# Optimization experiments

Measured on AMD Instinct MI355X. Metric: run time of the kernel, lower is better.

The kernel has to match this reference:

```python
import jax, jax.numpy as jnp
import numpy as np

B, S, E = 2, 2048, 2048
H, W = 16, 256  # num_heads, window_size
D = E // H      # head_dim = 128


def setup_inputs() -> dict:
    key = jax.random.key(0)
    ks = jax.random.split(key, 9)
    s = 1.0 / np.sqrt(E)
    return {
        "x": jax.random.normal(ks[0], (B, S, E), dtype=jnp.float32),
        "Wq": jax.random.normal(ks[1], (E, E), dtype=jnp.float32) * s,
        "bq": jax.random.normal(ks[2], (E,), dtype=jnp.float32) * 0.01,
        "Wk": jax.random.normal(ks[3], (E, E), dtype=jnp.float32) * s,
        "bk": jax.random.normal(ks[4], (E,), dtype=jnp.float32) * 0.01,
        "Wv": jax.random.normal(ks[5], (E, E), dtype=jnp.float32) * s,
        "bv": jax.random.normal(ks[6], (E,), dtype=jnp.float32) * 0.01,
        "Wo": jax.random.normal(ks[7], (E, E), dtype=jnp.float32) * s,
        "bo": jax.random.normal(ks[8], (E,), dtype=jnp.float32) * 0.01,
    }


def reference(x, Wq, bq, Wk, bk, Wv, bv, Wo, bo):
    Bsz, Sl, _ = x.shape
    # projections -> [B, H, S, D]
    def proj(Wt, bt):
        return (x @ Wt + bt).reshape(Bsz, Sl, H, D).transpose(0, 2, 1, 3)
    q = proj(Wq, bq)
    k = proj(Wk, bk)
    v = proj(Wv, bv)
    # scores [B, H, S, S]
    scores = jnp.einsum("bhqd,bhkd->bhqk", q, k) / jnp.sqrt(jnp.float32(D))
    # causal sliding-window mask: q_pos - W < k_pos <= q_pos
    q_pos = jnp.arange(Sl)[:, None]
    k_pos = jnp.arange(Sl)[None, :]
    valid = (k_pos <= q_pos) & (k_pos > q_pos - W)
    scores = jnp.where(valid, scores, jnp.float32(-jnp.inf))
    attn = jax.nn.softmax(scores, axis=-1)
    ctx = jnp.einsum("bhqk,bhkd->bhqd", attn, v)
    ctx = ctx.transpose(0, 2, 1, 3).reshape(Bsz, Sl, E)
    out = ctx @ Wo + bo
    return out, k, v
```

## Files before the change

### kernel.cpp

```cpp
#include <hip/hip_runtime.h>
#include <hip/hip_bf16.h>

#define SEQ 2048
#define EMB 2048
#define NH 16
#define WIN 256
#define HD 128
#define KDIM 2048
#define NDIM 2048

typedef __bf16 bf16x8 __attribute__((ext_vector_type(8)));
typedef float f32x4 __attribute__((ext_vector_type(4)));

#define MFMA __builtin_amdgcn_mfma_f32_16x16x32_bf16
#define BAR __builtin_amdgcn_s_barrier

__device__ __forceinline__ ushort f2bf(float f) {
  unsigned int x = __float_as_uint(f);
  unsigned int r = (x + 0x7fffu + ((x >> 16) & 1u)) >> 16;
  return (ushort)r;
}

__device__ __forceinline__ void gl16(const ushort* g, ushort* l) {
  __builtin_amdgcn_global_load_lds(
      (const __attribute__((address_space(1))) ushort*)g,
      (__attribute__((address_space(3))) ushort*)l, 16, 0, 0);
}

__global__ __launch_bounds__(256) void xconv_kernel(
    const float* __restrict__ x, ushort* __restrict__ xb) {
  size_t i = ((size_t)blockIdx.x * 256 + threadIdx.x) * 8;
  float4 f0 = *(const float4*)&x[i];
  float4 f1 = *(const float4*)&x[i + 4];
  union { ushort u[8]; uint4 v; } pk;
  pk.u[0] = f2bf(f0.x); pk.u[1] = f2bf(f0.y);
  pk.u[2] = f2bf(f0.z); pk.u[3] = f2bf(f0.w);
  pk.u[4] = f2bf(f1.x); pk.u[5] = f2bf(f1.y);
  pk.u[6] = f2bf(f1.z); pk.u[7] = f2bf(f1.w);
  *(uint4*)&xb[i] = pk.v;
}

__global__ __launch_bounds__(256) void wtrans_kernel(
    const float* __restrict__ w0, const float* __restrict__ w1,
    const float* __restrict__ w2, const float* __restrict__ w3,
    ushort* __restrict__ wt) {
  __shared__ __align__(16) float tf[32 * 132];
  const int t = threadIdx.x;
  const int nblk = blockIdx.x, kblk = blockIdx.y, mat = blockIdx.z;
  const float* Wp = mat == 0 ? w0 : mat == 1 ? w1 : mat == 2 ? w2 : w3;
  const int n0 = nblk * 128, k0 = kblk * 32;
#pragma unroll
  for (int p = 0; p < 4; ++p) {
    int kk = (t >> 5) + 8 * p;
    int nn = (t & 31) * 4;
    float4 v = *(const float4*)&Wp[(size_t)(k0 + kk) * NDIM + n0 + nn];
    *(float4*)&tf[kk * 132 + nn] = v;
  }
  __syncthreads();
  ushort* dst = wt + (size_t)mat * ((size_t)NDIM * KDIM) +
                (size_t)(nblk * 64 + kblk) * 4096;
#pragma unroll
  for (int p = 0; p < 2; ++p) {
    int idx = p * 256 + t;
    int r = idx >> 2, cs = idx & 3;
    int c = cs ^ ((r >> 1) & 3);
    union { ushort u[8]; uint4 v; } pk;
#pragma unroll
    for (int j = 0; j < 8; ++j) pk.u[j] = f2bf(tf[(c * 8 + j) * 132 + r]);
    *(uint4*)&dst[idx * 8] = pk.v;
  }
}

__global__ __launch_bounds__(256) void kvprep_kernel(
    const float* __restrict__ Kf, const float* __restrict__ Vf,
    ushort* __restrict__ Kb, ushort* __restrict__ vT) {
  __shared__ float tf[64 * 129];
  const int t = threadIdx.x;
  if (blockIdx.z == 1) {
    size_t base = ((size_t)(blockIdx.y * 32 + blockIdx.x)) * 8192;
#pragma unroll
    for (int p = 0; p < 4; ++p) {
      size_t i = base + p * 2048 + t * 8;
      float4 f0 = *(const float4*)&Kf[i];
      float4 f1 = *(const float4*)&Kf[i + 4];
      union { ushort u[8]; uint4 v; } pk;
      pk.u[0] = f2bf(f0.x); pk.u[1] = f2bf(f0.y);
      pk.u[2] = f2bf(f0.z); pk.u[3] = f2bf(f0.w);
      pk.u[4] = f2bf(f1.x); pk.u[5] = f2bf(f1.y);
      pk.u[6] = f2bf(f1.z); pk.u[7] = f2bf(f1.w);
      *(uint4*)&Kb[i] = pk.v;
    }
    return;
  }
  const int s0 = blockIdx.x * 64, bh = blockIdx.y;
  const float* src = Vf + ((size_t)bh * SEQ + s0) * HD;
#pragma unroll
  for (int p = 0; p < 8; ++p) {
    int idx = p * 256 + t;
    int s = idx >> 5, c4 = (idx & 31) * 4;
    float4 v = *(const float4*)&src[(size_t)s * HD + c4];
    float* d = &tf[s * 129 + c4];
    d[0] = v.x; d[1] = v.y; d[2] = v.z; d[3] = v.w;
  }
  __syncthreads();
  ushort* dst = vT + (size_t)bh * HD * SEQ + s0;
#pragma unroll
  for (int p = 0; p < 4; ++p) {
    int slot = p * 256 + t;
    int d = slot >> 3, c = slot & 7;
    union { ushort u[8]; uint4 v; } pk;
#pragma unroll
    for (int j = 0; j < 8; ++j) pk.u[j] = f2bf(tf[(c * 8 + j) * 129 + d]);
    *(uint4*)&dst[(size_t)d * SEQ + c * 8] = pk.v;
  }
}

template <int MODE>
__global__ __launch_bounds__(256) void gemm_kernel(
    const ushort* __restrict__ Ab, const ushort* __restrict__ Wt,
    const float* __restrict__ b0, const float* __restrict__ b1,
    const float* __restrict__ b2, float* __restrict__ outF,
    ushort* __restrict__ outQ) {
  __shared__ __align__(16) ushort As[128 * 32];
  __shared__ __align__(16) ushort Bs[128 * 32];
  const int t = threadIdx.x;
  const int mblk = blockIdx.x, nblk = blockIdx.y, z = blockIdx.z;
  const int m0 = mblk * 128, n0 = nblk * 128;
  const ushort* wtile = Wt + (size_t)z * ((size_t)NDIM * KDIM) +
                        (size_t)(nblk * 64) * 4096;
  const int lane = t & 63, wid = t >> 6;
  const int l15 = lane & 15, lg = lane >> 4;
  const int wm = wid >> 1, wn = wid & 1;
  f32x4 acc[4][4] = {};

  const int slot0 = wid * 128 + lane;
  const int slot1 = slot0 + 64;
  const int r0 = slot0 >> 2, c0 = (slot0 & 3) ^ ((r0 >> 1) & 3);
  const int r1 = slot1 >> 2, c1 = (slot1 & 3) ^ ((r1 >> 1) & 3);
  const ushort* aS0 = Ab + (size_t)(m0 + r0) * KDIM + c0 * 8;
  const ushort* aS1 = Ab + (size_t)(m0 + r1) * KDIM + c1 * 8;
  const ushort* bS0 = wtile + slot0 * 8;
  const ushort* bS1 = wtile + slot1 * 8;
  ushort* aD0 = &As[(wid * 128) * 8];
  ushort* aD1 = &As[(wid * 128 + 64) * 8];
  ushort* bD0 = &Bs[(wid * 128) * 8];
  ushort* bD1 = &Bs[(wid * 128 + 64) * 8];

  for (int kt = 0; kt < KDIM / 32; ++kt) {
    __syncthreads();
    gl16(aS0, aD0); gl16(aS1, aD1);
    gl16(bS0, bD0); gl16(bS1, bD1);
    aS0 += 32; aS1 += 32; bS0 += 4096; bS1 += 4096;
    __syncthreads();
    bf16x8 af[4], bfr[4];
#pragma unroll
    for (int mf = 0; mf < 4; ++mf) {
      int r = wm * 64 + mf * 16 + l15;
      af[mf] = *(const bf16x8*)&As[r * 32 + ((lg ^ ((r >> 1) & 3)) * 8)];
    }
#pragma unroll
    for (int nf = 0; nf < 4; ++nf) {
      int r = wn * 64 + nf * 16 + l15;
      bfr[nf] = *(const bf16x8*)&Bs[r * 32 + ((lg ^ ((r >> 1) & 3)) * 8)];
    }
#pragma unroll
    for (int mf = 0; mf < 4; ++mf)
#pragma unroll
      for (int nf = 0; nf < 4; ++nf)
        acc[mf][nf] = MFMA(af[mf], bfr[nf], acc[mf][nf], 0, 0, 0);
  }

  const float* bias = (MODE == 0) ? b0 : (z == 0 ? b0 : z == 1 ? b1 : b2);
#pragma unroll
  for (int nf = 0; nf < 4; ++nf) {
    int nl = wn * 64 + nf * 16 + l15;
    int n = n0 + nl;
    float bv = bias[n];
#pragma unroll
    for (int mf = 0; mf < 4; ++mf) {
#pragma unroll
      for (int r = 0; r < 4; ++r) {
        int m = m0 + wm * 64 + mf * 16 + lg * 4 + r;
        float val = acc[mf][nf][r] + bv;
        if (MODE == 0) {
          outF[(size_t)m * NDIM + n] = val;
        } else {
          int b = m >> 11, s = m & 2047;
          size_t idx = (((size_t)b * NH + nblk) * SEQ + s) * HD + nl;
          if (z == 0) outQ[idx] = f2bf(val);
          else outF[(z == 1 ? (size_t)8388608u : (size_t)16777216u) + idx] = val;
        }
      }
    }
  }
}

__global__ __launch_bounds__(256) void attn_kernel(
    const ushort* __restrict__ Qb, const ushort* __restrict__ Kb,
    const ushort* __restrict__ vT, ushort* __restrict__ ctx) {
  __shared__ __align__(16) ushort Kl[2][8192];
  __shared__ __align__(16) ushort Vt[2][8192];
  __shared__ __align__(16) ushort Pl[4608];
  const int t = threadIdx.x;
  const int bid = blockIdx.x;
  const int bh = (bid & 7) * 4 + (bid >> 8);
  const int q0 = ((bid >> 3) & 31) * 64;
  const int lane = t & 63, w = t >> 6;
  const int l15 = lane & 15, lg = lane >> 4;
  const int b = bh >> 4, h = bh & 15;
  const ushort* Qbase = Qb + (size_t)bh * SEQ * HD;
  const ushort* Kbase = Kb + (size_t)bh * SEQ * HD;
  const ushort* Vbase = vT + (size_t)bh * HD * SEQ;

  const ushort* kS[4];
  const ushort* vS[4];
#pragma unroll
  for (int p = 0; p < 4; ++p) {
    int s = p * 256 + t;
    int kr = s >> 4, kc = (s & 15) ^ (kr & 7);
    kS[p] = Kbase + kr * HD + kc * 8;
    int vr = s >> 3, vc = (s & 7) ^ (vr & 7);
    vS[p] = Vbase + vr * SEQ + vc * 8;
  }

#define ASTAGE(kt, buf)                                                  \
  {                                                                      \
    size_t ko = (size_t)(kt) * 8192, vo = (size_t)(kt) * 64;             \
    gl16(kS[0] + ko, &Kl[buf][(w * 64) * 8]);                            \
    gl16(kS[1] + ko, &Kl[buf][(256 + w * 64) * 8]);                      \
    gl16(kS[2] + ko, &Kl[buf][(512 + w * 64) * 8]);                      \
    gl16(kS[3] + ko, &Kl[buf][(768 + w * 64) * 8]);                      \
    gl16(vS[0] + vo, &Vt[buf][(w * 64) * 8]);                            \
    gl16(vS[1] + vo, &Vt[buf][(256 + w * 64) * 8]);                      \
    gl16(vS[2] + vo, &Vt[buf][(512 + w * 64) * 8]);                      \
    gl16(vS[3] + vo, &Vt[buf][(768 + w * 64) * 8]);                      \
  }

  bf16x8 aq[4];
#pragma unroll
  for (int ds = 0; ds < 4; ++ds)
    aq[ds] = *(const bf16x8*)&Qbase[(size_t)(q0 + w * 16 + l15) * HD + ds * 32 + lg * 8];

  f32x4 accc[8] = {};
  float mrow[4], lrow[4];
#pragma unroll
  for (int r = 0; r < 4; ++r) { mrow[r] = -1e30f; lrow[r] = 0.f; }

  int ktlo = (q0 - WIN + 1) >> 6;
  if (ktlo < 0) ktlo = 0;
  const int kthi = q0 >> 6;

  ASTAGE(ktlo, 0)
  {
    int t1 = (ktlo + 1 <= kthi) ? ktlo + 1 : kthi;
    ASTAGE(t1, 1)
  }

  for (int kt = ktlo; kt <= kthi; ++kt) {
    const int buf = (kt - ktlo) & 1;
    asm volatile("s_waitcnt vmcnt(8)" ::: "memory");
    BAR();

    f32x4 sacc[4] = {};
#pragma unroll
    for (int ds = 0; ds < 4; ++ds) {
#pragma unroll
      for (int kf = 0; kf < 4; ++kf) {
        int key = kf * 16 + l15;
        bf16x8 kb = *(const bf16x8*)&Kl[buf][key * 128 + (((ds * 4 + lg) ^ (key & 7)) * 8)];
        sacc[kf] = MFMA(aq[ds], kb, sacc[kf], 0, 0, 0);
      }
    }

    const float scale = 0.08838834764831845f;
    const float L2E = 1.4426950408889634f;
#pragma unroll
    for (int r = 0; r < 4; ++r) {
      int q = q0 + w * 16 + lg * 4 + r;
      float sv[4];
      float mx = -1e30f;
#pragma unroll
      for (int kf = 0; kf < 4; ++kf) {
        int key = kt * 64 + kf * 16 + l15;
        float s = sacc[kf][r] * scale;
        bool valid = (key <= q) && (key + WIN > q);
        s = valid ? s : -1e30f;
        sv[kf] = s;
        mx = fmaxf(mx, s);
      }
      mx = fmaxf(mx, __shfl_xor(mx, 1));
      mx = fmaxf(mx, __shfl_xor(mx, 2));
      mx = fmaxf(mx, __shfl_xor(mx, 4));
      mx = fmaxf(mx, __shfl_xor(mx, 8));
      float mnew = fmaxf(mrow[r], mx);
      float sf = exp2f((mrow[r] - mnew) * L2E);
      float ps = 0.f;
#pragma unroll
      for (int kf = 0; kf < 4; ++kf) {
        float p = (sv[kf] > -1e29f) ? exp2f((sv[kf] - mnew) * L2E) : 0.f;
        ps += p;
        Pl[w * 1152 + (lg * 4 + r) * 72 + kf * 16 + l15] = f2bf(p);
      }
      ps += __shfl_xor(ps, 1);
      ps += __shfl_xor(ps, 2);
      ps += __shfl_xor(ps, 4);
      ps += __shfl_xor(ps, 8);
      lrow[r] = lrow[r] * sf + ps;
      mrow[r] = mnew;
#pragma unroll
      for (int nf = 0; nf < 8; ++nf) accc[nf][r] *= sf;
    }

#pragma unroll
    for (int ks = 0; ks < 2; ++ks) {
      bf16x8 pa = *(const bf16x8*)&Pl[w * 1152 + l15 * 72 + ks * 32 + lg * 8];
#pragma unroll
      for (int nf = 0; nf < 8; ++nf) {
        int vr = nf * 16 + l15;
        bf16x8 vb = *(const bf16x8*)&Vt[buf][vr * 64 + (((ks * 4 + lg) ^ (vr & 7)) * 8)];
        accc[nf] = MFMA(pa, vb, accc[nf], 0, 0, 0);
      }
    }

    BAR();
    {
      int ts = (kt + 2 <= kthi) ? kt + 2 : kthi;
      ASTAGE(ts, buf)
    }
  }
#undef ASTAGE

#pragma unroll
  for (int r = 0; r < 4; ++r) {
    int q = q0 + w * 16 + lg * 4 + r;
    float inv = 1.0f / lrow[r];
    size_t rowoff = ((size_t)b * SEQ + q) * EMB + (size_t)h * HD;
#pragma unroll
    for (int nf = 0; nf < 8; ++nf)
      ctx[rowoff + nf * 16 + l15] = f2bf(accc[nf][r] * inv);
  }
}

extern "C" void kernel_launch(void* const* d_in, const int* in_sizes, int n_in,
                              void* d_out, int out_size, void* d_ws, size_t ws_size,
                              hipStream_t stream) {
  const float* x  = (const float*)d_in[0];
  const float* Wq = (const float*)d_in[1];
  const float* bq = (const float*)d_in[2];
  const float* Wk = (const float*)d_in[3];
  const float* bk = (const float*)d_in[4];
  const float* Wv = (const float*)d_in[5];
  const float* bv = (const float*)d_in[6];
  const float* Wo = (const float*)d_in[7];
  const float* bo = (const float*)d_in[8];
  float* out = (float*)d_out;
  ushort* ws = (ushort*)d_ws;
  ushort* Wt   = ws;
  ushort* Qb   = ws + 16777216;
  ushort* Kbf  = ws + 25165824;
  ushort* vTb  = ws + 33554432;
  ushort* xb   = ws + 41943040;
  ushort* ctxb = xb;

  xconv_kernel<<<4096, 256, 0, stream>>>(x, xb);
  wtrans_kernel<<<dim3(16, 64, 4), 256, 0, stream>>>(Wq, Wk, Wv, Wo, Wt);
  gemm_kernel<1><<<dim3(32, 16, 3), 256, 0, stream>>>(xb, Wt, bq, bk, bv, out, Qb);
  kvprep_kernel<<<dim3(32, 32, 2), 256, 0, stream>>>(out + 8388608,
                                                     out + 16777216, Kbf, vTb);
  attn_kernel<<<1024, 256, 0, stream>>>(Qb, Kbf, vTb, ctxb);
  gemm_kernel<0><<<dim3(32, 16, 1), 256, 0, stream>>>(
      ctxb, Wt + (size_t)3 * 4194304, bo, nullptr, nullptr, out, nullptr);
}
```

Before: 245.9 us.

## Fuse x conversion into weight prep kernel; load K/V directly from global in attention

```diff
diff --git a/kernel.cpp b/kernel.cpp
--- a/kernel.cpp
+++ b/kernel.cpp
@@ -13,7 +13,6 @@
 typedef float f32x4 __attribute__((ext_vector_type(4)));
 
 #define MFMA __builtin_amdgcn_mfma_f32_16x16x32_bf16
-#define BAR __builtin_amdgcn_s_barrier
 
 __device__ __forceinline__ ushort f2bf(float f) {
   unsigned int x = __float_as_uint(f);
@@ -27,25 +26,29 @@
       (__attribute__((address_space(3))) ushort*)l, 16, 0, 0);
 }
 
-__global__ __launch_bounds__(256) void xconv_kernel(
-    const float* __restrict__ x, ushort* __restrict__ xb) {
-  size_t i = ((size_t)blockIdx.x * 256 + threadIdx.x) * 8;
-  float4 f0 = *(const float4*)&x[i];
-  float4 f1 = *(const float4*)&x[i + 4];
-  union { ushort u[8]; uint4 v; } pk;
-  pk.u[0] = f2bf(f0.x); pk.u[1] = f2bf(f0.y);
-  pk.u[2] = f2bf(f0.z); pk.u[3] = f2bf(f0.w);
-  pk.u[4] = f2bf(f1.x); pk.u[5] = f2bf(f1.y);
-  pk.u[6] = f2bf(f1.z); pk.u[7] = f2bf(f1.w);
-  *(uint4*)&xb[i] = pk.v;
-}
-
-__global__ __launch_bounds__(256) void wtrans_kernel(
-    const float* __restrict__ w0, const float* __restrict__ w1,
-    const float* __restrict__ w2, const float* __restrict__ w3,
+__global__ __launch_bounds__(256) void prep_kernel(
+    const float* __restrict__ x, const float* __restrict__ w0,
+    const float* __restrict__ w1, const float* __restrict__ w2,
+    const float* __restrict__ w3, ushort* __restrict__ xb,
     ushort* __restrict__ wt) {
+  const int t = threadIdx.x;
+  if (blockIdx.z == 4) {
+    int bid = blockIdx.y * 16 + blockIdx.x;
+#pragma unroll
+    for (int p = 0; p < 4; ++p) {
+      size_t i = (((size_t)bid * 4 + p) * 256 + t) * 8;
+      float4 f0 = *(const float4*)&x[i];
+      float4 f1 = *(const float4*)&x[i + 4];
+      union { ushort u[8]; uint4 v; } pk;
+      pk.u[0] = f2bf(f0.x); pk.u[1] = f2bf(f0.y);
+      pk.u[2] = f2bf(f0.z); pk.u[3] = f2bf(f0.w);
+      pk.u[4] = f2bf(f1.x); pk.u[5] = f2bf(f1.y);
+      pk.u[6] = f2bf(f1.z); pk.u[7] = f2bf(f1.w);
+      *(uint4*)&xb[i] = pk.v;
+    }
+    return;
+  }
   __shared__ __align__(16) float tf[32 * 132];
-  const int t = threadIdx.x;
   const int nblk = blockIdx.x, kblk = blockIdx.y, mat = blockIdx.z;
   const float* Wp = mat == 0 ? w0 : mat == 1 ? w1 : mat == 2 ? w2 : w3;
   const int n0 = nblk * 128, k0 = kblk * 32;
@@ -198,8 +201,6 @@
 __global__ __launch_bounds__(256) void attn_kernel(
     const ushort* __restrict__ Qb, const ushort* __restrict__ Kb,
     const ushort* __restrict__ vT, ushort* __restrict__ ctx) {
-  __shared__ __align__(16) ushort Kl[2][8192];
-  __shared__ __align__(16) ushort Vt[2][8192];
   __shared__ __align__(16) ushort Pl[4608];
   const int t = threadIdx.x;
   const int bid = blockIdx.x;
@@ -212,30 +213,6 @@
   const ushort* Kbase = Kb + (size_t)bh * SEQ * HD;
   const ushort* Vbase = vT + (size_t)bh * HD * SEQ;
 
-  const ushort* kS[4];
-  const ushort* vS[4];
-#pragma unroll
-  for (int p = 0; p < 4; ++p) {
-    int s = p * 256 + t;
-    int kr = s >> 4, kc = (s & 15) ^ (kr & 7);
-    kS[p] = Kbase + kr * HD + kc * 8;
-    int vr = s >> 3, vc = (s & 7) ^ (vr & 7);
-    vS[p] = Vbase + vr * SEQ + vc * 8;
-  }
-
-#define ASTAGE(kt, buf)                                                  \
-  {                                                                      \
-    size_t ko = (size_t)(kt) * 8192, vo = (size_t)(kt) * 64;             \
-    gl16(kS[0] + ko, &Kl[buf][(w * 64) * 8]);                            \
-    gl16(kS[1] + ko, &Kl[buf][(256 + w * 64) * 8]);                      \
-    gl16(kS[2] + ko, &Kl[buf][(512 + w * 64) * 8]);                      \
-    gl16(kS[3] + ko, &Kl[buf][(768 + w * 64) * 8]);                      \
-    gl16(vS[0] + vo, &Vt[buf][(w * 64) * 8]);                            \
-    gl16(vS[1] + vo, &Vt[buf][(256 + w * 64) * 8]);                      \
-    gl16(vS[2] + vo, &Vt[buf][(512 + w * 64) * 8]);                      \
-    gl16(vS[3] + vo, &Vt[buf][(768 + w * 64) * 8]);                      \
-  }
-
   bf16x8 aq[4];
 #pragma unroll
   for (int ds = 0; ds < 4; ++ds)
@@ -250,24 +227,14 @@
   if (ktlo < 0) ktlo = 0;
   const int kthi = q0 >> 6;
 
-  ASTAGE(ktlo, 0)
-  {
-    int t1 = (ktlo + 1 <= kthi) ? ktlo + 1 : kthi;
-    ASTAGE(t1, 1)
-  }
-
   for (int kt = ktlo; kt <= kthi; ++kt) {
-    const int buf = (kt - ktlo) & 1;
-    asm volatile("s_waitcnt vmcnt(8)" ::: "memory");
-    BAR();
-
     f32x4 sacc[4] = {};
 #pragma unroll
     for (int ds = 0; ds < 4; ++ds) {
 #pragma unroll
       for (int kf = 0; kf < 4; ++kf) {
-        int key = kf * 16 + l15;
-        bf16x8 kb = *(const bf16x8*)&Kl[buf][key * 128 + (((ds * 4 + lg) ^ (key & 7)) * 8)];
+        bf16x8 kb = *(const bf16x8*)&Kbase[(size_t)(kt * 64 + kf * 16 + l15) * HD +
+                                           (ds * 4 + lg) * 8];
         sacc[kf] = MFMA(aq[ds], kb, sacc[kf], 0, 0, 0);
       }
     }
@@ -316,19 +283,12 @@
       bf16x8 pa = *(const bf16x8*)&Pl[w * 1152 + l15 * 72 + ks * 32 + lg * 8];
 #pragma unroll
       for (int nf = 0; nf < 8; ++nf) {
-        int vr = nf * 16 + l15;
-        bf16x8 vb = *(const bf16x8*)&Vt[buf][vr * 64 + (((ks * 4 + lg) ^ (vr & 7)) * 8)];
+        bf16x8 vb = *(const bf16x8*)&Vbase[(size_t)(nf * 16 + l15) * SEQ +
+                                           kt * 64 + (ks * 4 + lg) * 8];
         accc[nf] = MFMA(pa, vb, accc[nf], 0, 0, 0);
       }
     }
-
-    BAR();
-    {
-      int ts = (kt + 2 <= kthi) ? kt + 2 : kthi;
-      ASTAGE(ts, buf)
-    }
-  }
-#undef ASTAGE
+  }
 
 #pragma unroll
   for (int r = 0; r < 4; ++r) {
@@ -362,8 +322,7 @@
   ushort* xb   = ws + 41943040;
   ushort* ctxb = xb;
 
-  xconv_kernel<<<4096, 256, 0, stream>>>(x, xb);
-  wtrans_kernel<<<dim3(16, 64, 4), 256, 0, stream>>>(Wq, Wk, Wv, Wo, Wt);
+  prep_kernel<<<dim3(16, 64, 5), 256, 0, stream>>>(x, Wq, Wk, Wv, Wo, xb, Wt);
   gemm_kernel<1><<<dim3(32, 16, 3), 256, 0, stream>>>(xb, Wt, bq, bk, bv, out, Qb);
   kvprep_kernel<<<dim3(32, 32, 2), 256, 0, stream>>>(out + 8388608,
                                                      out + 16777216, Kbf, vTb);
```

Result: slower. 280.5 us (+14.1%).
